# Kernel tuning notes

Hardware: AMD Instinct MI355X
Metric: run time of the kernel (lower is better)

## Reference

```python
import jax, jax.numpy as jnp
import numpy as np

NUM_QUANTIZERS = 8


def setup_inputs() -> dict:
    key = jax.random.key(0)
    k1, k2 = jax.random.split(key)
    B, W, C = 16, 2048, 512
    Q, K = NUM_QUANTIZERS, 1024
    x = jax.random.normal(k1, (B, W, C), dtype=jnp.float32)
    # per-stage codebooks (shared_codebook=False), xavier-normal-ish scale
    codebooks = jax.random.normal(k2, (Q, K, C), dtype=jnp.float32) * (2.0 / (K + C)) ** 0.5
    return {"x": x, "codebooks": codebooks}


def reference(x, codebooks):
    """Residual quantization: per-stage cdist+argmin+lookup+residual update.

    x: [B, W, C] encoder latents; codebooks: [Q, K, C].
    Returns (final_z_q [B*W, C], commitment_loss scalar) — final_z_q is
    sum over quantizer stages of the straight-through quantized outputs
    (is_train=True path).
    """
    B, W, C = x.shape
    first_z_e = x.reshape(B * W, C)            # (b w) c
    z_e = first_z_e
    z_d = jnp.zeros_like(first_z_e)
    quant_sum = jnp.zeros_like(first_z_e)
    q_latent = jnp.float32(0.0)
    e_latent = jnp.float32(0.0)
    rq_latent = jnp.float32(0.0)
    for i in range(codebooks.shape[0]):
        cb = codebooks[i]                      # [K, C]
        # squared euclidean distances (argmin-equivalent to torch.cdist)
        dist2 = (jnp.sum(z_e * z_e, axis=1, keepdims=True)
                 - 2.0 * (z_e @ cb.T)
                 + jnp.sum(cb * cb, axis=1))   # [N, K]
        idx = jnp.argmin(dist2, axis=1)        # [N]
        z_q = cb[idx]                          # codebook lookup, [N, C]
        z_d = z_d + jax.lax.stop_gradient(z_q)
        q_latent = q_latent + jnp.mean((jax.lax.stop_gradient(z_e) - z_q) ** 2)
        e_latent = e_latent + jnp.mean((z_e - jax.lax.stop_gradient(z_q)) ** 2)
        rq_latent = rq_latent + jnp.mean((first_z_e - z_d) ** 2)
        # straight-through estimator (is_train=True)
        z_q_st = z_e + jax.lax.stop_gradient(z_q - z_e)
        quant_sum = quant_sum + z_q_st
        z_e = z_e - z_q_st
    commitment_loss = 0.75 * q_latent + e_latent + rq_latent
    return quant_sum, commitment_loss
```

## Files before the change

kernel.cpp:

```cpp
#include <hip/hip_runtime.h>

#define N_ROWS 32768
#define C_DIM  512
#define K_CODES 1024
#define Q_STAGES 8

typedef __attribute__((ext_vector_type(8))) short bf16x8;
typedef __attribute__((ext_vector_type(4))) float f32x4;
typedef __attribute__((ext_vector_type(4))) unsigned short u16x4;
typedef __attribute__((ext_vector_type(8))) unsigned short u16x8;

#define ZEH_OFF 0ull
#define ZEL_OFF 33554432ull
#define CBH_OFF 67108864ull
#define CBL_OFF 68157440ull
#define C2_OFF  69206016ull
#define IDX_OFF 69238784ull
#define RPT_OFF 69304320ull
#define LSB_OFF 69312512ull

#define GLD(gp, lp) __builtin_amdgcn_global_load_lds( \
    (const __attribute__((address_space(1))) void*)(gp), \
    (__attribute__((address_space(3))) void*)(lp), 16, 0, 0)

__device__ __forceinline__ float bf_hi_f(float f) {
    return __uint_as_float(__float_as_uint(f) & 0xFFFF0000u);
}
__device__ __forceinline__ unsigned short bf_hi_u(float f) {
    return (unsigned short)(__float_as_uint(f) >> 16);
}
__device__ __forceinline__ float u2f(unsigned short u) {
    return __uint_as_float(((unsigned int)u) << 16);
}

__global__ __launch_bounds__(256) void split_kernel(
    const float* __restrict__ src, unsigned short* __restrict__ h,
    unsigned short* __restrict__ l, int n4)
{
    int i = blockIdx.x * 256 + threadIdx.x;
    if (i >= n4) return;
    float4 v = *(const float4*)(src + (size_t)i * 4);
    u16x4 hv, lv;
    float f, hf;
    f = v.x; hv[0] = bf_hi_u(f); hf = bf_hi_f(f); lv[0] = bf_hi_u(f - hf);
    f = v.y; hv[1] = bf_hi_u(f); hf = bf_hi_f(f); lv[1] = bf_hi_u(f - hf);
    f = v.z; hv[2] = bf_hi_u(f); hf = bf_hi_f(f); lv[2] = bf_hi_u(f - hf);
    f = v.w; hv[3] = bf_hi_u(f); hf = bf_hi_f(f); lv[3] = bf_hi_u(f - hf);
    *(u16x4*)(h + (size_t)i * 4) = hv;
    *(u16x4*)(l + (size_t)i * 4) = lv;
}

__global__ __launch_bounds__(256) void rowsq_kernel(
    const float* __restrict__ src, float* __restrict__ dst, int nrows)
{
    int wave = (blockIdx.x * blockDim.x + threadIdx.x) >> 6;
    int lane = threadIdx.x & 63;
    if (wave >= nrows) return;
    const float* p = src + (size_t)wave * C_DIM + lane * 8;
    float4 a = *(const float4*)p;
    float4 b = *(const float4*)(p + 4);
    float s = a.x*a.x + a.y*a.y + a.z*a.z + a.w*a.w
            + b.x*b.x + b.y*b.y + b.z*b.z + b.w*b.w;
    #pragma unroll
    for (int off = 1; off < 64; off <<= 1) s += __shfl_xor(s, off);
    if (lane == 0) dst[wave] = s;
}

#define DBM2 128
#define DBNC 256
#define DBK 32
#define NSTEPS 64

__global__ __launch_bounds__(512, 2) void dist_kernel(
    const unsigned short* __restrict__ zeh, const unsigned short* __restrict__ zel,
    const unsigned short* __restrict__ cbh, const unsigned short* __restrict__ cbl,
    const float* __restrict__ c2s, unsigned short* __restrict__ idx_out)
{
    __shared__ unsigned short sA[3][2][DBM2 * DBK];
    __shared__ unsigned short sB[3][2][DBNC * DBK];
    __shared__ float c2_lds[K_CODES];

    const int tid  = threadIdx.x;
    const int lane = tid & 63;
    const int w    = tid >> 6;
    const int wr   = w >> 2;
    const int wc   = w & 3;
    const int lr   = lane & 15;
    const int kg   = lane >> 4;
    const int row0 = blockIdx.x * DBM2;

    for (int i = tid; i < K_CODES; i += 512) c2_lds[i] = c2s[i];

    const int srow = lane >> 2;
    const int scol = (((lane & 3) ^ ((srow >> 1) & 3))) * 8;
    const int aslot = (kg ^ ((lr >> 1) & 3)) * 8;

    float rbv[4][4];
    int   rbi[4][4];
    #pragma unroll
    for (int i = 0; i < 4; ++i)
        #pragma unroll
        for (int r = 0; r < 4; ++r) { rbv[i][r] = 3.4e38f; rbi[i][r] = 0x7fffffff; }

    f32x4 acc[4][4];
    #pragma unroll
    for (int i = 0; i < 4; ++i)
        #pragma unroll
        for (int j = 0; j < 4; ++j) acc[i][j] = (f32x4)0.f;

    auto stage = [&](int t, int b) {
        const int col0 = (t >> 4) * DBNC;
        const int kk = (t & 15) * DBK;
        GLD(zeh + (size_t)(row0 + w * 16 + srow) * C_DIM + kk + scol,
            &sA[b][0][(w * 16) * DBK]);
        GLD(zel + (size_t)(row0 + w * 16 + srow) * C_DIM + kk + scol,
            &sA[b][1][(w * 16) * DBK]);
        #pragma unroll
        for (int u = 0; u < 2; ++u) {
            const int rB = w * 32 + u * 16;
            GLD(cbh + (size_t)(col0 + rB + srow) * C_DIM + kk + scol,
                &sB[b][0][rB * DBK]);
            GLD(cbl + (size_t)(col0 + rB + srow) * C_DIM + kk + scol,
                &sB[b][1][rB * DBK]);
        }
    };

    __syncthreads();
    stage(0, 0);
    stage(1, 1);

    int cur = 0;
    #pragma unroll 1
    for (int t = 0; t < NSTEPS; ++t) {
        if (t == NSTEPS - 1) {
            asm volatile("s_waitcnt vmcnt(0)" ::: "memory");
        } else {
            asm volatile("s_waitcnt vmcnt(6)" ::: "memory");
        }
        __builtin_amdgcn_s_barrier();

        bf16x8 ah[4], al[4], bh[4], bl[4];
        #pragma unroll
        for (int mi = 0; mi < 4; ++mi) {
            const int rowoff = (wr * 64 + mi * 16 + lr) * DBK + aslot;
            ah[mi] = *(const bf16x8*)&sA[cur][0][rowoff];
        }
        #pragma unroll
        for (int ni = 0; ni < 4; ++ni) {
            const int rowoff = (wc * 64 + ni * 16 + lr) * DBK + aslot;
            bh[ni] = *(const bf16x8*)&sB[cur][0][rowoff];
        }
        __builtin_amdgcn_sched_barrier(0);
        #pragma unroll
        for (int ni = 0; ni < 4; ++ni) {
            const int rowoff = (wc * 64 + ni * 16 + lr) * DBK + aslot;
            bl[ni] = *(const bf16x8*)&sB[cur][1][rowoff];
        }
        #pragma unroll
        for (int mi = 0; mi < 4; ++mi) {
            const int rowoff = (wr * 64 + mi * 16 + lr) * DBK + aslot;
            al[mi] = *(const bf16x8*)&sA[cur][1][rowoff];
        }
        if (t < NSTEPS - 2) {
            int nxt = cur + 2; if (nxt > 2) nxt -= 3;
            stage(t + 2, nxt);
        }
        __builtin_amdgcn_sched_barrier(0);

        __builtin_amdgcn_s_setprio(1);
        #pragma unroll
        for (int mi = 0; mi < 4; ++mi)
            #pragma unroll
            for (int ni = 0; ni < 4; ++ni)
                acc[mi][ni] = __builtin_amdgcn_mfma_f32_16x16x32_bf16(
                    ah[mi], bh[ni], acc[mi][ni], 0, 0, 0);
        __builtin_amdgcn_s_setprio(0);
        __builtin_amdgcn_sched_barrier(0);

        __builtin_amdgcn_s_setprio(1);
        #pragma unroll
        for (int mi = 0; mi < 4; ++mi)
            #pragma unroll
            for (int ni = 0; ni < 4; ++ni)
                acc[mi][ni] = __builtin_amdgcn_mfma_f32_16x16x32_bf16(
                    ah[mi], bl[ni], acc[mi][ni], 0, 0, 0);
        __builtin_amdgcn_s_setprio(0);
        __builtin_amdgcn_sched_barrier(0);

        __builtin_amdgcn_s_setprio(1);
        #pragma unroll
        for (int mi = 0; mi < 4; ++mi)
            #pragma unroll
            for (int ni = 0; ni < 4; ++ni)
                acc[mi][ni] = __builtin_amdgcn_mfma_f32_16x16x32_bf16(
                    al[mi], bh[ni], acc[mi][ni], 0, 0, 0);
        __builtin_amdgcn_s_setprio(0);

        if ((t & 15) == 15) {
            const int col0 = (t >> 4) * DBNC;
            #pragma unroll
            for (int ni = 0; ni < 4; ++ni) {
                const int code = col0 + wc * 64 + ni * 16 + lr;
                const float c2v = c2_lds[code];
                #pragma unroll
                for (int mi = 0; mi < 4; ++mi)
                    #pragma unroll
                    for (int r = 0; r < 4; ++r) {
                        float d = fmaf(-2.f, acc[mi][ni][r], c2v);
                        if (d < rbv[mi][r]) { rbv[mi][r] = d; rbi[mi][r] = code; }
                    }
            }
            #pragma unroll
            for (int i = 0; i < 4; ++i)
                #pragma unroll
                for (int j = 0; j < 4; ++j) acc[i][j] = (f32x4)0.f;
        }

        cur = (cur == 2) ? 0 : cur + 1;
    }

    #pragma unroll
    for (int off = 1; off < 16; off <<= 1) {
        #pragma unroll
        for (int mi = 0; mi < 4; ++mi)
            #pragma unroll
            for (int r = 0; r < 4; ++r) {
                float ov = __shfl_xor(rbv[mi][r], off);
                int   oi = __shfl_xor(rbi[mi][r], off);
                if (ov < rbv[mi][r] || (ov == rbv[mi][r] && oi < rbi[mi][r])) {
                    rbv[mi][r] = ov; rbi[mi][r] = oi;
                }
            }
    }

    __syncthreads();
    float (*s_v)[4] = (float (*)[4])&sA[0][0][0];
    int   (*s_i)[4] = (int (*)[4])((char*)&sA[0][0][0] + DBM2 * 4 * 4);
    if (lr == 0) {
        #pragma unroll
        for (int mi = 0; mi < 4; ++mi)
            #pragma unroll
            for (int r = 0; r < 4; ++r) {
                int lrow = wr * 64 + mi * 16 + kg * 4 + r;
                s_v[lrow][wc] = rbv[mi][r];
                s_i[lrow][wc] = rbi[mi][r];
            }
    }
    __syncthreads();
    if (tid < DBM2) {
        float bv = s_v[tid][0]; int bi = s_i[tid][0];
        #pragma unroll
        for (int c = 1; c < 4; ++c) {
            float v = s_v[tid][c]; int i = s_i[tid][c];
            if (v < bv || (v == bv && i < bi)) { bv = v; bi = i; }
        }
        idx_out[row0 + tid] = (unsigned short)bi;
    }
}

__global__ __launch_bounds__(1024) void update_kernel(
    const int s, const float* __restrict__ x, const float* __restrict__ cb,
    const unsigned short* __restrict__ idx_sel, float* __restrict__ out,
    unsigned short* __restrict__ zeh, unsigned short* __restrict__ zel,
    float* __restrict__ rpart)
{
    __shared__ float swsum[16];
    const int wid = threadIdx.x >> 6, lane = threadIdx.x & 63;
    const int r = blockIdx.x * 16 + wid;
    const int bi = idx_sel[r];
    const size_t base = (size_t)r * C_DIM + lane * 8;
    const float* q = cb + (size_t)bi * C_DIM + lane * 8;

    float4 q0 = *(const float4*)q;
    float4 q1 = *(const float4*)(q + 4);
    float qq[8] = {q0.x, q0.y, q0.z, q0.w, q1.x, q1.y, q1.z, q1.w};

    float v[8];
    if (s == 0) {
        float4 z0 = *(const float4*)(x + base);
        float4 z1 = *(const float4*)(x + base + 4);
        v[0]=z0.x; v[1]=z0.y; v[2]=z0.z; v[3]=z0.w;
        v[4]=z1.x; v[5]=z1.y; v[6]=z1.z; v[7]=z1.w;
    } else {
        u16x8 h = *(const u16x8*)(zeh + base);
        u16x8 l = *(const u16x8*)(zel + base);
        #pragma unroll
        for (int j = 0; j < 8; ++j) v[j] = u2f(h[j]) + u2f(l[j]);
    }

    float rr[8];
    #pragma unroll
    for (int j = 0; j < 8; ++j) rr[j] = v[j] - qq[j];

    if (s < Q_STAGES - 1) {
        u16x8 hh, ll;
        #pragma unroll
        for (int j = 0; j < 8; ++j) {
            hh[j] = bf_hi_u(rr[j]);
            float lo = rr[j] - bf_hi_f(rr[j]);
            ll[j] = bf_hi_u(lo);
        }
        *(u16x8*)(zeh + base) = hh;
        *(u16x8*)(zel + base) = ll;
    } else {
        float4 x0 = *(const float4*)(x + base);
        float4 x1 = *(const float4*)(x + base + 4);
        float4 o0, o1;
        o0.x = x0.x - rr[0]; o0.y = x0.y - rr[1];
        o0.z = x0.z - rr[2]; o0.w = x0.w - rr[3];
        o1.x = x1.x - rr[4]; o1.y = x1.y - rr[5];
        o1.z = x1.z - rr[6]; o1.w = x1.w - rr[7];
        *(float4*)(out + base)     = o0;
        *(float4*)(out + base + 4) = o1;
    }

    float ssum = 0.f;
    #pragma unroll
    for (int j = 0; j < 8; ++j) ssum += rr[j] * rr[j];
    #pragma unroll
    for (int off = 1; off < 64; off <<= 1) ssum += __shfl_xor(ssum, off);
    if (lane == 0) swsum[wid] = ssum;
    __syncthreads();
    if (threadIdx.x == 0) {
        float t = 0.f;
        #pragma unroll
        for (int i = 0; i < 16; ++i) t += swsum[i];
        rpart[blockIdx.x] = t;
    }
}

__global__ __launch_bounds__(1024) void reduce2048_kernel(
    const float* __restrict__ rpart, float* __restrict__ slot)
{
    __shared__ float sm[1024];
    int t = threadIdx.x;
    sm[t] = rpart[t] + rpart[t + 1024];
    __syncthreads();
    for (int w2 = 512; w2 > 0; w2 >>= 1) {
        if (t < w2) sm[t] += sm[t + w2];
        __syncthreads();
    }
    if (t == 0) *slot = sm[0];
}

__global__ void finalize_kernel(const float* __restrict__ lossbuf,
                                float* __restrict__ out)
{
    if (threadIdx.x == 0) {
        float s = 0.f;
        #pragma unroll
        for (int i = 0; i < Q_STAGES; ++i) s += lossbuf[i];
        out[0] = 2.75f * s / (float)((size_t)N_ROWS * C_DIM);
    }
}

extern "C" void kernel_launch(void* const* d_in, const int* in_sizes, int n_in,
                              void* d_out, int out_size, void* d_ws, size_t ws_size,
                              hipStream_t stream)
{
    const float* x   = (const float*)d_in[0];
    const float* cbs = (const float*)d_in[1];
    float* out = (float*)d_out;
    char* ws = (char*)d_ws;

    unsigned short* zeh = (unsigned short*)(ws + ZEH_OFF);
    unsigned short* zel = (unsigned short*)(ws + ZEL_OFF);
    unsigned short* cbh = (unsigned short*)(ws + CBH_OFF);
    unsigned short* cbl = (unsigned short*)(ws + CBL_OFF);
    float* c2    = (float*)(ws + C2_OFF);
    unsigned short* gidx = (unsigned short*)(ws + IDX_OFF);
    float* rpart = (float*)(ws + RPT_OFF);
    float* lossb = (float*)(ws + LSB_OFF);

    split_kernel<<<(N_ROWS * C_DIM / 4 + 255) / 256, 256, 0, stream>>>(
        x, zeh, zel, N_ROWS * C_DIM / 4);
    rowsq_kernel<<<(Q_STAGES * K_CODES * 64) / 256, 256, 0, stream>>>(
        cbs, c2, Q_STAGES * K_CODES);

    for (int s = 0; s < Q_STAGES; ++s) {
        const float* cb = cbs + (size_t)s * K_CODES * C_DIM;
        split_kernel<<<(K_CODES * C_DIM / 4 + 255) / 256, 256, 0, stream>>>(
            cb, cbh, cbl, K_CODES * C_DIM / 4);
        dist_kernel<<<N_ROWS / DBM2, 512, 0, stream>>>(
            zeh, zel, cbh, cbl, c2 + (size_t)s * K_CODES, gidx);
        update_kernel<<<N_ROWS / 16, 1024, 0, stream>>>(
            s, x, cb, gidx, out, zeh, zel, rpart);
        reduce2048_kernel<<<1, 1024, 0, stream>>>(rpart, lossb + s);
    }
    finalize_kernel<<<1, 64, 0, stream>>>(lossb, out + (size_t)N_ROWS * C_DIM);
}
```

Before: 1.015 ms.

## Software-pipeline LDS fragment loads in dist kernel and fuse per-stage small kernels

The distance GEMM loop is reorganised so the high-half A/B fragments for the next K-step are read from LDS at the end of the current iteration. The low-half loads are interleaved between MFMA groups, with extra barriers separating the phases, so LDS reads overlap with matrix work. The per-stage codebook bf16 split is folded into extra blocks of the update kernel, which prepare the next stage's codebook. The per-stage loss reductions are merged into one final kernel. Together these drop about two launches per stage, in exchange for more barriers per iteration and a larger workspace region for the partial sums.

```diff
diff --git a/kernel.cpp b/kernel.cpp
--- a/kernel.cpp
+++ b/kernel.cpp
@@ -17,7 +17,6 @@
 #define C2_OFF  69206016ull
 #define IDX_OFF 69238784ull
 #define RPT_OFF 69304320ull
-#define LSB_OFF 69312512ull
 
 #define GLD(gp, lp) __builtin_amdgcn_global_load_lds( \
     (const __attribute__((address_space(1))) void*)(gp), \
@@ -128,45 +127,29 @@
     __syncthreads();
     stage(0, 0);
     stage(1, 1);
+    asm volatile("s_waitcnt vmcnt(6)" ::: "memory");
+    __builtin_amdgcn_s_barrier();
+
+    bf16x8 ah[4], al[4], bh[4], bl[4];
+    #pragma unroll
+    for (int mi = 0; mi < 4; ++mi)
+        ah[mi] = *(const bf16x8*)&sA[0][0][(wr * 64 + mi * 16 + lr) * DBK + aslot];
+    #pragma unroll
+    for (int ni = 0; ni < 4; ++ni)
+        bh[ni] = *(const bf16x8*)&sB[0][0][(wc * 64 + ni * 16 + lr) * DBK + aslot];
 
     int cur = 0;
     #pragma unroll 1
     for (int t = 0; t < NSTEPS; ++t) {
-        if (t == NSTEPS - 1) {
-            asm volatile("s_waitcnt vmcnt(0)" ::: "memory");
-        } else {
-            asm volatile("s_waitcnt vmcnt(6)" ::: "memory");
-        }
-        __builtin_amdgcn_s_barrier();
-
-        bf16x8 ah[4], al[4], bh[4], bl[4];
-        #pragma unroll
-        for (int mi = 0; mi < 4; ++mi) {
-            const int rowoff = (wr * 64 + mi * 16 + lr) * DBK + aslot;
-            ah[mi] = *(const bf16x8*)&sA[cur][0][rowoff];
-        }
-        #pragma unroll
-        for (int ni = 0; ni < 4; ++ni) {
-            const int rowoff = (wc * 64 + ni * 16 + lr) * DBK + aslot;
-            bh[ni] = *(const bf16x8*)&sB[cur][0][rowoff];
-        }
-        __builtin_amdgcn_sched_barrier(0);
-        #pragma unroll
-        for (int ni = 0; ni < 4; ++ni) {
-            const int rowoff = (wc * 64 + ni * 16 + lr) * DBK + aslot;
-            bl[ni] = *(const bf16x8*)&sB[cur][1][rowoff];
-        }
-        #pragma unroll
-        for (int mi = 0; mi < 4; ++mi) {
-            const int rowoff = (wr * 64 + mi * 16 + lr) * DBK + aslot;
-            al[mi] = *(const bf16x8*)&sA[cur][1][rowoff];
-        }
-        if (t < NSTEPS - 2) {
-            int nxt = cur + 2; if (nxt > 2) nxt -= 3;
-            stage(t + 2, nxt);
-        }
-        __builtin_amdgcn_sched_barrier(0);
-
+        const int nxt = (cur == 2) ? 0 : cur + 1;
+        const int n2  = (nxt == 2) ? 0 : nxt + 1;
+
+        asm volatile("s_waitcnt lgkmcnt(0)" ::: "memory");
+        __builtin_amdgcn_sched_barrier(0);
+        #pragma unroll
+        for (int ni = 0; ni < 4; ++ni)
+            bl[ni] = *(const bf16x8*)&sB[cur][1][(wc * 64 + ni * 16 + lr) * DBK + aslot];
+        __builtin_amdgcn_sched_barrier(0);
         __builtin_amdgcn_s_setprio(1);
         #pragma unroll
         for (int mi = 0; mi < 4; ++mi)
@@ -176,7 +159,20 @@
                     ah[mi], bh[ni], acc[mi][ni], 0, 0, 0);
         __builtin_amdgcn_s_setprio(0);
         __builtin_amdgcn_sched_barrier(0);
-
+        __builtin_amdgcn_s_barrier();
+
+        asm volatile("s_waitcnt lgkmcnt(0)" ::: "memory");
+        __builtin_amdgcn_sched_barrier(0);
+        #pragma unroll
+        for (int mi = 0; mi < 4; ++mi)
+            al[mi] = *(const bf16x8*)&sA[cur][1][(wr * 64 + mi * 16 + lr) * DBK + aslot];
+        if (t < NSTEPS - 2) stage(t + 2, n2);
+        if (t <= NSTEPS - 3) {
+            asm volatile("s_waitcnt vmcnt(6)" ::: "memory");
+        } else {
+            asm volatile("s_waitcnt vmcnt(0)" ::: "memory");
+        }
+        __builtin_amdgcn_sched_barrier(0);
         __builtin_amdgcn_s_setprio(1);
         #pragma unroll
         for (int mi = 0; mi < 4; ++mi)
@@ -186,7 +182,10 @@
                     ah[mi], bl[ni], acc[mi][ni], 0, 0, 0);
         __builtin_amdgcn_s_setprio(0);
         __builtin_amdgcn_sched_barrier(0);
-
+        __builtin_amdgcn_s_barrier();
+
+        asm volatile("s_waitcnt lgkmcnt(0)" ::: "memory");
+        __builtin_amdgcn_sched_barrier(0);
         __builtin_amdgcn_s_setprio(1);
         #pragma unroll
         for (int mi = 0; mi < 4; ++mi)
@@ -195,7 +194,15 @@
                 acc[mi][ni] = __builtin_amdgcn_mfma_f32_16x16x32_bf16(
                     al[mi], bh[ni], acc[mi][ni], 0, 0, 0);
         __builtin_amdgcn_s_setprio(0);
-
+        __builtin_amdgcn_sched_barrier(0);
+        if (t < NSTEPS - 1) {
+            #pragma unroll
+            for (int mi = 0; mi < 4; ++mi)
+                ah[mi] = *(const bf16x8*)&sA[nxt][0][(wr * 64 + mi * 16 + lr) * DBK + aslot];
+            #pragma unroll
+            for (int ni = 0; ni < 4; ++ni)
+                bh[ni] = *(const bf16x8*)&sB[nxt][0][(wc * 64 + ni * 16 + lr) * DBK + aslot];
+        }
         if ((t & 15) == 15) {
             const int col0 = (t >> 4) * DBNC;
             #pragma unroll
@@ -215,8 +222,8 @@
                 #pragma unroll
                 for (int j = 0; j < 4; ++j) acc[i][j] = (f32x4)0.f;
         }
-
-        cur = (cur == 2) ? 0 : cur + 1;
+        __builtin_amdgcn_s_barrier();
+        cur = nxt;
     }
 
     #pragma unroll
@@ -260,10 +267,25 @@
 
 __global__ __launch_bounds__(1024) void update_kernel(
     const int s, const float* __restrict__ x, const float* __restrict__ cb,
-    const unsigned short* __restrict__ idx_sel, float* __restrict__ out,
-    unsigned short* __restrict__ zeh, unsigned short* __restrict__ zel,
-    float* __restrict__ rpart)
-{
+    const float* __restrict__ cb_next, const unsigned short* __restrict__ idx_sel,
+    float* __restrict__ out, unsigned short* __restrict__ zeh,
+    unsigned short* __restrict__ zel, unsigned short* __restrict__ cbh,
+    unsigned short* __restrict__ cbl, float* __restrict__ rpart)
+{
+    if (blockIdx.x >= 2048) {
+        int i = (blockIdx.x - 2048) * 1024 + threadIdx.x;
+        float4 v = *(const float4*)(cb_next + (size_t)i * 4);
+        u16x4 hv, lv;
+        float f, hf;
+        f = v.x; hv[0] = bf_hi_u(f); hf = bf_hi_f(f); lv[0] = bf_hi_u(f - hf);
+        f = v.y; hv[1] = bf_hi_u(f); hf = bf_hi_f(f); lv[1] = bf_hi_u(f - hf);
+        f = v.z; hv[2] = bf_hi_u(f); hf = bf_hi_f(f); lv[2] = bf_hi_u(f - hf);
+        f = v.w; hv[3] = bf_hi_u(f); hf = bf_hi_f(f); lv[3] = bf_hi_u(f - hf);
+        *(u16x4*)(cbh + (size_t)i * 4) = hv;
+        *(u16x4*)(cbl + (size_t)i * 4) = lv;
+        return;
+    }
+
     __shared__ float swsum[16];
     const int wid = threadIdx.x >> 6, lane = threadIdx.x & 63;
     const int r = blockIdx.x * 16 + wid;
@@ -329,29 +351,23 @@
     }
 }
 
-__global__ __launch_bounds__(1024) void reduce2048_kernel(
-    const float* __restrict__ rpart, float* __restrict__ slot)
+__global__ __launch_bounds__(1024) void finalize_all_kernel(
+    const float* __restrict__ rpart, float* __restrict__ out_loss)
 {
     __shared__ float sm[1024];
-    int t = threadIdx.x;
-    sm[t] = rpart[t] + rpart[t + 1024];
-    __syncthreads();
-    for (int w2 = 512; w2 > 0; w2 >>= 1) {
-        if (t < w2) sm[t] += sm[t + w2];
+    const int t = threadIdx.x;
+    float tot = 0.f;
+    for (int s = 0; s < Q_STAGES; ++s) {
+        sm[t] = rpart[s * 2048 + t] + rpart[s * 2048 + 1024 + t];
         __syncthreads();
-    }
-    if (t == 0) *slot = sm[0];
-}
-
-__global__ void finalize_kernel(const float* __restrict__ lossbuf,
-                                float* __restrict__ out)
-{
-    if (threadIdx.x == 0) {
-        float s = 0.f;
-        #pragma unroll
-        for (int i = 0; i < Q_STAGES; ++i) s += lossbuf[i];
-        out[0] = 2.75f * s / (float)((size_t)N_ROWS * C_DIM);
-    }
+        for (int w2 = 512; w2 > 0; w2 >>= 1) {
+            if (t < w2) sm[t] += sm[t + w2];
+            __syncthreads();
+        }
+        if (t == 0) tot += sm[0];
+        __syncthreads();
+    }
+    if (t == 0) out_loss[0] = 2.75f * tot / (float)((size_t)N_ROWS * C_DIM);
 }
 
 extern "C" void kernel_launch(void* const* d_in, const int* in_sizes, int n_in,
@@ -370,22 +386,22 @@
     float* c2    = (float*)(ws + C2_OFF);
     unsigned short* gidx = (unsigned short*)(ws + IDX_OFF);
     float* rpart = (float*)(ws + RPT_OFF);
-    float* lossb = (float*)(ws + LSB_OFF);
 
     split_kernel<<<(N_ROWS * C_DIM / 4 + 255) / 256, 256, 0, stream>>>(
         x, zeh, zel, N_ROWS * C_DIM / 4);
+    split_kernel<<<(K_CODES * C_DIM / 4 + 255) / 256, 256, 0, stream>>>(
+        cbs, cbh, cbl, K_CODES * C_DIM / 4);
     rowsq_kernel<<<(Q_STAGES * K_CODES * 64) / 256, 256, 0, stream>>>(
         cbs, c2, Q_STAGES * K_CODES);
 
     for (int s = 0; s < Q_STAGES; ++s) {
-        const float* cb = cbs + (size_t)s * K_CODES * C_DIM;
-        split_kernel<<<(K_CODES * C_DIM / 4 + 255) / 256, 256, 0, stream>>>(
-            cb, cbh, cbl, K_CODES * C_DIM / 4);
+        const float* cb  = cbs + (size_t)s * K_CODES * C_DIM;
+        const float* cbn = (s < Q_STAGES - 1) ? cb + (size_t)K_CODES * C_DIM : cbs;
         dist_kernel<<<N_ROWS / DBM2, 512, 0, stream>>>(
             zeh, zel, cbh, cbl, c2 + (size_t)s * K_CODES, gidx);
-        update_kernel<<<N_ROWS / 16, 1024, 0, stream>>>(
-            s, x, cb, gidx, out, zeh, zel, rpart);
-        reduce2048_kernel<<<1, 1024, 0, stream>>>(rpart, lossb + s);
-    }
-    finalize_kernel<<<1, 64, 0, stream>>>(lossb, out + (size_t)N_ROWS * C_DIM);
-}
+        const int nblk = (s < Q_STAGES - 1) ? 2048 + 128 : 2048;
+        update_kernel<<<nblk, 1024, 0, stream>>>(
+            s, x, cb, cbn, gidx, out, zeh, zel, cbh, cbl, rpart + s * 2048);
+    }
+    finalize_all_kernel<<<1, 1024, 0, stream>>>(rpart, out + (size_t)N_ROWS * C_DIM);
+}
```

After: 1.184 ms. 16.6% more time.
